# Optimization experiments

Measured on AMD Instinct MI355X. Metric: run time of the kernel, lower is better.

The kernel has to match this reference:

```python
import jax, jax.numpy as jnp
import numpy as np

H, KVH, DH = 16, 4, 128
EPS = 1e-8

def _rmsnorm(t, gamma):
    # normalize over last dim (dim_head)
    ms = jnp.mean(t * t, axis=-1, keepdims=True)
    return t * jax.lax.rsqrt(ms + EPS) * gamma

def setup_inputs() -> dict:
    key = jax.random.key(0)
    ks = jax.random.split(key, 5)
    d = H * DH  # 2048
    kv_d = KVH * DH  # 512
    x = jax.random.normal(ks[0], (2, 2048, d), dtype=jnp.float32)
    Wq = jax.random.normal(ks[1], (d, d), dtype=jnp.float32) * (d ** -0.5)
    Wk = jax.random.normal(ks[2], (d, kv_d), dtype=jnp.float32) * (d ** -0.5)
    Wv = jax.random.normal(ks[3], (d, kv_d), dtype=jnp.float32) * (d ** -0.5)
    Wo = jax.random.normal(ks[4], (d, d), dtype=jnp.float32) * (d ** -0.5)
    q_gamma = jnp.ones((DH,), dtype=jnp.float32)
    k_gamma = jnp.ones((DH,), dtype=jnp.float32)
    return {"x": x, "Wq": Wq, "Wk": Wk, "Wv": Wv, "Wo": Wo,
            "q_gamma": q_gamma, "k_gamma": k_gamma}

def reference(x, Wq, Wk, Wv, Wo, q_gamma, k_gamma):
    b, s, d = x.shape
    g = H // KVH  # GQA group size
    q = (x @ Wq).reshape(b, s, H, DH)
    k = (x @ Wk).reshape(b, s, KVH, DH)
    v = (x @ Wv).reshape(b, s, KVH, DH)
    # fused QK RMSNorm (per-head, over dim_head)
    q = _rmsnorm(q, q_gamma)
    k = _rmsnorm(k, k_gamma)
    # GQA: expand kv heads across query-head groups
    k = jnp.repeat(k, g, axis=2)  # [b, s, H, DH]
    v = jnp.repeat(v, g, axis=2)
    scores = jnp.einsum('bqhd,bkhd->bhqk', q, k) * (DH ** -0.5)
    causal = jnp.tril(jnp.ones((s, s), dtype=bool))
    scores = jnp.where(causal, scores, jnp.finfo(scores.dtype).min)
    attn = jax.nn.softmax(scores, axis=-1)
    out = jnp.einsum('bhqk,bkhd->bqhd', attn, v).reshape(b, s, H * DH)
    out = out @ Wo
    return out + x  # residual skip
```

## Files before the change

kernel.cpp:

```cpp
#include <hip/hip_runtime.h>

typedef unsigned short u16;
typedef __attribute__((ext_vector_type(8))) short short8;
typedef __attribute__((ext_vector_type(4))) float f32x4;

#define DEVI __device__ __forceinline__

DEVI float u2f(u16 u) {
    unsigned int x = ((unsigned int)u) << 16;
    float f; __builtin_memcpy(&f, &x, 4); return f;
}
DEVI u16 f2u(float f) {
    unsigned int x; __builtin_memcpy(&x, &f, 4);
    x = (x + 0x7fffu + ((x >> 16) & 1u)) >> 16;
    return (u16)x;
}
DEVI unsigned int fbits(float f) {
    unsigned int x; __builtin_memcpy(&x, &f, 4); return x;
}
DEVI void gld16(const u16* g, u16* ldsbase) {
    __builtin_amdgcn_global_load_lds(
        (const __attribute__((address_space(1))) unsigned int*)g,
        (__attribute__((address_space(3))) unsigned int*)ldsbase, 16, 0, 0);
}

__global__ __launch_bounds__(256) void prep(
    const float* __restrict__ x,
    const float* __restrict__ Wq, const float* __restrict__ Wk,
    const float* __restrict__ Wv, const float* __restrict__ Wo,
    u16* __restrict__ xbf, u16* __restrict__ WTqkv, u16* __restrict__ WoT)
{
    __shared__ u16 T[64 * 72];
    int id = blockIdx.x;
    const int tid = threadIdx.x;
    if (id < 4096) {
        int g = (id * 256 + tid) * 8;
        float4 a = *(const float4*)&x[g];
        float4 c = *(const float4*)&x[g + 4];
        short8 v;
        v[0]=(short)f2u(a.x); v[1]=(short)f2u(a.y); v[2]=(short)f2u(a.z); v[3]=(short)f2u(a.w);
        v[4]=(short)f2u(c.x); v[5]=(short)f2u(c.y); v[6]=(short)f2u(c.z); v[7]=(short)f2u(c.w);
        *(short8*)&xbf[g] = v;
        return;
    }
    id -= 4096;
    const float* W; u16* WT; int N, bx, by;
    if (id < 1024)      {            W = Wo; WT = WoT;   N = 2048; bx = id & 31; by = id >> 5; }
    else if (id < 2048) { id -= 1024; W = Wq; WT = WTqkv; N = 2048; bx = id & 31; by = id >> 5; }
    else if (id < 2304) { id -= 2048; W = Wk; WT = WTqkv + (size_t)2048 * 2048; N = 512; bx = id & 7; by = id >> 3; }
    else                { id -= 2304; W = Wv; WT = WTqkv + (size_t)2560 * 2048; N = 512; bx = id & 7; by = id >> 3; }
    const int K = 2048;
    const int k0 = by * 64, n0 = bx * 64;
#pragma unroll
    for (int i = 0; i < 2; ++i) {
        int c = tid + i * 256;
        int row = c >> 3, n8 = (c & 7) * 8;
        const float* src = &W[(size_t)(k0 + row) * N + n0 + n8];
#pragma unroll
        for (int j = 0; j < 8; ++j)
            T[(n8 + j) * 72 + row] = f2u(src[j]);
    }
    __syncthreads();
#pragma unroll
    for (int i = 0; i < 2; ++i) {
        int c = tid + i * 256;
        int n = c >> 3, k8 = (c & 7) * 8;
        *(short8*)&WT[(size_t)(n0 + n) * K + k0 + k8] = *(const short8*)&T[n * 72 + k8];
    }
}

__global__ __launch_bounds__(256) void gemm_lds(
    const u16* __restrict__ A, int lda,
    const u16* __restrict__ WT,
    void* __restrict__ C, int ldc, const float* __restrict__ resid, int c_f32,
    int M, int N, int K,
    const float* __restrict__ qg, const float* __restrict__ kg, int fuse_norm)
{
    __shared__ u16 As[128 * 32];
    __shared__ u16 Bs[128 * 32];
    const int tid = threadIdx.x;
    const int lane = tid & 63, w = tid >> 6;
    const int wm = w >> 1, wn = w & 1;
    const int l15 = lane & 15, quad = lane >> 4;
    const int r4 = lane >> 2, c4 = (lane & 3) * 8;
    const int m0 = blockIdx.y * 128, n0 = blockIdx.x * 128;

    f32x4 acc[4][4] = {};
    for (int k0 = 0; k0 < K; k0 += 32) {
#pragma unroll
        for (int j = 0; j < 2; ++j) {
            int row = w * 32 + j * 16;
            gld16(&WT[(size_t)(n0 + row + r4) * K + k0 + c4], &Bs[row * 32]);
            gld16(&A [(size_t)(m0 + row + r4) * lda + k0 + c4], &As[row * 32]);
        }
        __syncthreads();
        short8 a[4], b[4];
#pragma unroll
        for (int mt = 0; mt < 4; ++mt)
            a[mt] = *(const short8*)&As[(wm * 64 + mt * 16 + l15) * 32 + quad * 8];
#pragma unroll
        for (int nt = 0; nt < 4; ++nt)
            b[nt] = *(const short8*)&Bs[(wn * 64 + nt * 16 + l15) * 32 + quad * 8];
#pragma unroll
        for (int mt = 0; mt < 4; ++mt)
#pragma unroll
            for (int nt = 0; nt < 4; ++nt)
                acc[mt][nt] = __builtin_amdgcn_mfma_f32_16x16x32_bf16(a[mt], b[nt], acc[mt][nt], 0, 0, 0);
        __syncthreads();
    }

    if (fuse_norm && n0 < 2560) {
        const float* gamma = (n0 < 2048) ? qg : kg;
        float* red = (float*)As;
#pragma unroll
        for (int mt = 0; mt < 4; ++mt)
#pragma unroll
            for (int r = 0; r < 4; ++r) {
                float p = 0.f;
#pragma unroll
                for (int nt = 0; nt < 4; ++nt) p += acc[mt][nt][r] * acc[mt][nt][r];
#pragma unroll
                for (int msk = 1; msk < 16; msk <<= 1) p += __shfl_xor(p, msk);
                if (l15 == 0)
                    red[(wm * 64 + mt * 16 + quad * 4 + r) * 2 + wn] = p;
            }
        __syncthreads();
        float gv[4];
#pragma unroll
        for (int nt = 0; nt < 4; ++nt) gv[nt] = gamma[wn * 64 + nt * 16 + l15];
#pragma unroll
        for (int mt = 0; mt < 4; ++mt)
#pragma unroll
            for (int r = 0; r < 4; ++r) {
                int rl = wm * 64 + mt * 16 + quad * 4 + r;
                float m2 = red[rl * 2] + red[rl * 2 + 1];
                float sc = rsqrtf(m2 * (1.0f / 128.0f) + 1e-8f);
#pragma unroll
                for (int nt = 0; nt < 4; ++nt) acc[mt][nt][r] *= sc * gv[nt];
            }
    }

#pragma unroll
    for (int mt = 0; mt < 4; ++mt) {
#pragma unroll
        for (int r = 0; r < 4; ++r) {
            int row = m0 + wm * 64 + mt * 16 + quad * 4 + r;
#pragma unroll
            for (int nt = 0; nt < 4; ++nt) {
                int col = n0 + wn * 64 + nt * 16 + l15;
                float v = acc[mt][nt][r];
                if (resid) v += resid[(size_t)row * ldc + col];
                if (c_f32) ((float*)C)[(size_t)row * ldc + col] = v;
                else       ((u16*)C)[(size_t)row * ldc + col] = f2u(v);
            }
        }
    }
}

__global__ __launch_bounds__(256) void vtrans(
    const u16* __restrict__ qkv, u16* __restrict__ vT)
{
    __shared__ u16 T[128 * 72];
    const int tid = threadIdx.x;
    const int t0 = blockIdx.x * 64;
    const int kvh = blockIdx.y, b = blockIdx.z;
#pragma unroll
    for (int i = 0; i < 4; ++i) {
        int c = tid + i * 256;
        int tl = c >> 4, d8 = (c & 15) * 8;
        short8 v = *(const short8*)&qkv[(size_t)(b * 2048 + t0 + tl) * 3072 + 2560 + kvh * 128 + d8];
#pragma unroll
        for (int j = 0; j < 8; ++j)
            T[(d8 + j) * 72 + tl] = (u16)v[j];
    }
    __syncthreads();
#pragma unroll
    for (int i = 0; i < 4; ++i) {
        int c = tid + i * 256;
        int d = c >> 3, t8 = (c & 7) * 8;
        *(short8*)&vT[((size_t)(b * 4 + kvh) * 128 + d) * 2048 + t0 + t8] =
            *(const short8*)&T[d * 72 + t8];
    }
}

#define QS 136
#define VS 72
__global__ __launch_bounds__(256) void attn(
    u16* __restrict__ qkv, const u16* __restrict__ vT)
{
    __shared__ u16 lds[17920];
    u16* const Ks = lds;
    u16* const Vs = lds + 8704;

    const int tid = threadIdx.x, lane = tid & 63, w = tid >> 6;
    const int l15 = lane & 15, quad = lane >> 4;
    const int h = blockIdx.y, b = blockIdx.z;
    const int kvh = h >> 2;
    const int qts[2] = { (int)blockIdx.x, 31 - (int)blockIdx.x };
    const float scale = 0.08838834764831845f;

#pragma unroll
    for (int t = 0; t < 2; ++t)
#pragma unroll
        for (int i = 0; i < 4; ++i) {
            int c = tid + i * 256;
            int r = c >> 4, d8 = (c & 15) * 8;
            *(short8*)&lds[t * 8704 + r * QS + d8] =
                *(const short8*)&qkv[(size_t)(b * 2048 + qts[t] * 64 + r) * 3072 + h * 128 + d8];
        }
    __syncthreads();
    short8 qf[2][4];
#pragma unroll
    for (int t = 0; t < 2; ++t)
#pragma unroll
        for (int ks = 0; ks < 4; ++ks)
            qf[t][ks] = *(const short8*)&lds[t * 8704 + (w * 16 + l15) * QS + ks * 32 + quad * 8];
    __syncthreads();

    f32x4 o[2][8] = {};
    float m_[2] = { -1e30f, -1e30f }, l_[2] = { 0.f, 0.f };

    for (int kt = 0; kt <= qts[1]; ++kt) {
        const int kv0 = kt * 64;
#pragma unroll
        for (int i = 0; i < 4; ++i) {
            int c = tid + i * 256;
            int r = c >> 4, d8 = (c & 15) * 8;
            *(short8*)&Ks[r * QS + d8] =
                *(const short8*)&qkv[(size_t)(b * 2048 + kv0 + r) * 3072 + 2048 + kvh * 128 + d8];
        }
#pragma unroll
        for (int i = 0; i < 4; ++i) {
            int c = tid + i * 256;
            int d = c >> 3, t8 = (c & 7) * 8;
            *(short8*)&Vs[d * VS + t8] =
                *(const short8*)&vT[((size_t)(b * 4 + kvh) * 128 + d) * 2048 + kv0 + t8];
        }
        __syncthreads();

#pragma unroll
        for (int t = 0; t < 2; ++t) {
            if (kt > qts[t]) continue;
            f32x4 s[4];
#pragma unroll
            for (int nt = 0; nt < 4; ++nt) {
                f32x4 a = {};
#pragma unroll
                for (int ks = 0; ks < 4; ++ks) {
                    short8 kf = *(const short8*)&Ks[(nt * 16 + l15) * QS + ks * 32 + quad * 8];
                    a = __builtin_amdgcn_mfma_f32_16x16x32_bf16(kf, qf[t][ks], a, 0, 0, 0);
                }
                s[nt] = a;
            }
            if (kt == qts[t]) {
                int qrow = w * 16 + l15;
#pragma unroll
                for (int nt = 0; nt < 4; ++nt)
#pragma unroll
                    for (int r = 0; r < 4; ++r) {
                        float v = s[nt][r] * scale;
                        if (nt * 16 + quad * 4 + r > qrow) v = -1e30f;
                        s[nt][r] = v;
                    }
            } else {
#pragma unroll
                for (int nt = 0; nt < 4; ++nt)
#pragma unroll
                    for (int r = 0; r < 4; ++r) s[nt][r] *= scale;
            }
            float mx = s[0][0];
#pragma unroll
            for (int nt = 0; nt < 4; ++nt)
#pragma unroll
                for (int r = 0; r < 4; ++r) mx = fmaxf(mx, s[nt][r]);
            mx = fmaxf(mx, __shfl_xor(mx, 16));
            mx = fmaxf(mx, __shfl_xor(mx, 32));
            float mn = fmaxf(m_[t], mx);
            float alpha = __expf(m_[t] - mn);
            m_[t] = mn;
            float sum = 0.f;
#pragma unroll
            for (int nt = 0; nt < 4; ++nt)
#pragma unroll
                for (int r = 0; r < 4; ++r) {
                    float p = __expf(s[nt][r] - mn);
                    s[nt][r] = p;
                    sum += p;
                }
            sum += __shfl_xor(sum, 16);
            sum += __shfl_xor(sum, 32);
            l_[t] = l_[t] * alpha + sum;
            unsigned int pk[4][2];
#pragma unroll
            for (int nt = 0; nt < 4; ++nt)
#pragma unroll
                for (int i = 0; i < 2; ++i)
                    pk[nt][i] = __builtin_amdgcn_perm(
                        fbits(s[nt][2 * i + 1]), fbits(s[nt][2 * i]), 0x07060302u);
            int af[2][4];
#pragma unroll
            for (int c = 0; c < 2; ++c)
#pragma unroll
                for (int d = 0; d < 4; ++d) {
                    int src = l15 + 16 * ((quad & 1) * 2 + (d >> 1));
                    int v0 = __shfl((int)pk[2 * c][d & 1], src);
                    int v1 = __shfl((int)pk[2 * c + 1][d & 1], src);
                    af[c][d] = (quad >= 2) ? v1 : v0;
                }
            union { int i4[4]; short8 s8; } ua0, ua1;
#pragma unroll
            for (int d = 0; d < 4; ++d) { ua0.i4[d] = af[0][d]; ua1.i4[d] = af[1][d]; }
#pragma unroll
            for (int r = 0; r < 4; ++r) {
                float ao = __shfl(alpha, quad * 4 + r);
#pragma unroll
                for (int nto = 0; nto < 8; ++nto) o[t][nto][r] *= ao;
            }
#pragma unroll
            for (int nto = 0; nto < 8; ++nto) {
                short8 bv0 = *(const short8*)&Vs[(nto * 16 + l15) * VS + quad * 8];
                short8 bv1 = *(const short8*)&Vs[(nto * 16 + l15) * VS + 32 + quad * 8];
                o[t][nto] = __builtin_amdgcn_mfma_f32_16x16x32_bf16(ua0.s8, bv0, o[t][nto], 0, 0, 0);
                o[t][nto] = __builtin_amdgcn_mfma_f32_16x16x32_bf16(ua1.s8, bv1, o[t][nto], 0, 0, 0);
            }
        }
        __syncthreads();
    }
#pragma unroll
    for (int t = 0; t < 2; ++t) {
        float rl = 1.0f / l_[t];
#pragma unroll
        for (int r = 0; r < 4; ++r) {
            float inv = __shfl(rl, quad * 4 + r);
            int row = qts[t] * 64 + w * 16 + quad * 4 + r;
#pragma unroll
            for (int nto = 0; nto < 8; ++nto)
                qkv[(size_t)(b * 2048 + row) * 3072 + h * 128 + nto * 16 + l15] =
                    f2u(o[t][nto][r] * inv);
        }
    }
}

extern "C" void kernel_launch(void* const* d_in, const int* in_sizes, int n_in,
                              void* d_out, int out_size, void* d_ws, size_t ws_size,
                              hipStream_t stream) {
    const float* x  = (const float*)d_in[0];
    const float* Wq = (const float*)d_in[1];
    const float* Wk = (const float*)d_in[2];
    const float* Wv = (const float*)d_in[3];
    const float* Wo = (const float*)d_in[4];
    const float* qg = (const float*)d_in[5];
    const float* kg = (const float*)d_in[6];

    char* ws = (char*)d_ws;
    u16* WoT   = (u16*)(ws);
    u16* QKV   = (u16*)(ws + 8388608);
    u16* vT    = (u16*)(ws + 33554432);
    u16* WTqkv = (u16*)(ws + 33554432);
    u16* xbf   = (u16*)d_out;

    prep<<<dim3(6656), 256, 0, stream>>>(x, Wq, Wk, Wv, Wo, xbf, WTqkv, WoT);

    gemm_lds<<<dim3(24, 32), 256, 0, stream>>>(xbf, 2048, WTqkv, QKV, 3072,
                                               nullptr, 0, 4096, 3072, 2048,
                                               qg, kg, 1);

    vtrans<<<dim3(32, 4, 2), 256, 0, stream>>>(QKV, vT);

    attn<<<dim3(16, 16, 2), 256, 0, stream>>>(QKV, vT);

    gemm_lds<<<dim3(16, 32), 256, 0, stream>>>(QKV, 3072, WoT, d_out, 2048,
                                               x, 1, 4096, 2048, 2048,
                                               nullptr, nullptr, 0);
}
```

Measured before the change: 357.9 us.

## Split paired causal query tiles into one tile per attention block

The attention kernel previously had each block handle two query tiles (qt and 31-qt) to balance causal work and share each K/V tile load between them. It now launches twice as many blocks, each handling one query tile, with a swizzled tile index that mixes short and long blocks across heads and batches. This doubles the number of blocks available to fill the GPU's compute units and halves per-block register use for the accumulators. In exchange, every K/V tile is loaded once per query tile instead of once per pair, and per-block work becomes imbalanced, leaving it to the scheduler to even out.

```diff
diff --git a/kernel.cpp b/kernel.cpp
--- a/kernel.cpp
+++ b/kernel.cpp
@@ -196,31 +196,27 @@
     const int l15 = lane & 15, quad = lane >> 4;
     const int h = blockIdx.y, b = blockIdx.z;
     const int kvh = h >> 2;
-    const int qts[2] = { (int)blockIdx.x, 31 - (int)blockIdx.x };
+    const int qt = ((int)blockIdx.x + ((h >> 3) << 3) + (b << 4)) & 31;
     const float scale = 0.08838834764831845f;
 
 #pragma unroll
-    for (int t = 0; t < 2; ++t)
-#pragma unroll
-        for (int i = 0; i < 4; ++i) {
-            int c = tid + i * 256;
-            int r = c >> 4, d8 = (c & 15) * 8;
-            *(short8*)&lds[t * 8704 + r * QS + d8] =
-                *(const short8*)&qkv[(size_t)(b * 2048 + qts[t] * 64 + r) * 3072 + h * 128 + d8];
-        }
+    for (int i = 0; i < 4; ++i) {
+        int c = tid + i * 256;
+        int r = c >> 4, d8 = (c & 15) * 8;
+        *(short8*)&Ks[r * QS + d8] =
+            *(const short8*)&qkv[(size_t)(b * 2048 + qt * 64 + r) * 3072 + h * 128 + d8];
+    }
     __syncthreads();
-    short8 qf[2][4];
-#pragma unroll
-    for (int t = 0; t < 2; ++t)
-#pragma unroll
-        for (int ks = 0; ks < 4; ++ks)
-            qf[t][ks] = *(const short8*)&lds[t * 8704 + (w * 16 + l15) * QS + ks * 32 + quad * 8];
+    short8 qf[4];
+#pragma unroll
+    for (int ks = 0; ks < 4; ++ks)
+        qf[ks] = *(const short8*)&Ks[(w * 16 + l15) * QS + ks * 32 + quad * 8];
     __syncthreads();
 
-    f32x4 o[2][8] = {};
-    float m_[2] = { -1e30f, -1e30f }, l_[2] = { 0.f, 0.f };
-
-    for (int kt = 0; kt <= qts[1]; ++kt) {
+    f32x4 o[8] = {};
+    float m_ = -1e30f, l_ = 0.f;
+
+    for (int kt = 0; kt <= qt; ++kt) {
         const int kv0 = kt * 64;
 #pragma unroll
         for (int i = 0; i < 4; ++i) {
@@ -238,105 +234,100 @@
         }
         __syncthreads();
 
-#pragma unroll
-        for (int t = 0; t < 2; ++t) {
-            if (kt > qts[t]) continue;
-            f32x4 s[4];
-#pragma unroll
-            for (int nt = 0; nt < 4; ++nt) {
-                f32x4 a = {};
-#pragma unroll
-                for (int ks = 0; ks < 4; ++ks) {
-                    short8 kf = *(const short8*)&Ks[(nt * 16 + l15) * QS + ks * 32 + quad * 8];
-                    a = __builtin_amdgcn_mfma_f32_16x16x32_bf16(kf, qf[t][ks], a, 0, 0, 0);
+        f32x4 s[4];
+#pragma unroll
+        for (int nt = 0; nt < 4; ++nt) {
+            f32x4 a = {};
+#pragma unroll
+            for (int ks = 0; ks < 4; ++ks) {
+                short8 kf = *(const short8*)&Ks[(nt * 16 + l15) * QS + ks * 32 + quad * 8];
+                a = __builtin_amdgcn_mfma_f32_16x16x32_bf16(kf, qf[ks], a, 0, 0, 0);
+            }
+            s[nt] = a;
+        }
+        if (kt == qt) {
+            int qrow = w * 16 + l15;
+#pragma unroll
+            for (int nt = 0; nt < 4; ++nt)
+#pragma unroll
+                for (int r = 0; r < 4; ++r) {
+                    float v = s[nt][r] * scale;
+                    if (nt * 16 + quad * 4 + r > qrow) v = -1e30f;
+                    s[nt][r] = v;
                 }
-                s[nt] = a;
-            }
-            if (kt == qts[t]) {
-                int qrow = w * 16 + l15;
-#pragma unroll
-                for (int nt = 0; nt < 4; ++nt)
-#pragma unroll
-                    for (int r = 0; r < 4; ++r) {
-                        float v = s[nt][r] * scale;
-                        if (nt * 16 + quad * 4 + r > qrow) v = -1e30f;
-                        s[nt][r] = v;
-                    }
-            } else {
-#pragma unroll
-                for (int nt = 0; nt < 4; ++nt)
-#pragma unroll
-                    for (int r = 0; r < 4; ++r) s[nt][r] *= scale;
-            }
-            float mx = s[0][0];
+        } else {
 #pragma unroll
             for (int nt = 0; nt < 4; ++nt)
 #pragma unroll
-                for (int r = 0; r < 4; ++r) mx = fmaxf(mx, s[nt][r]);
-            mx = fmaxf(mx, __shfl_xor(mx, 16));
-            mx = fmaxf(mx, __shfl_xor(mx, 32));
-            float mn = fmaxf(m_[t], mx);
-            float alpha = __expf(m_[t] - mn);
-            m_[t] = mn;
-            float sum = 0.f;
-#pragma unroll
-            for (int nt = 0; nt < 4; ++nt)
-#pragma unroll
-                for (int r = 0; r < 4; ++r) {
-                    float p = __expf(s[nt][r] - mn);
-                    s[nt][r] = p;
-                    sum += p;
-                }
-            sum += __shfl_xor(sum, 16);
-            sum += __shfl_xor(sum, 32);
-            l_[t] = l_[t] * alpha + sum;
-            unsigned int pk[4][2];
-#pragma unroll
-            for (int nt = 0; nt < 4; ++nt)
-#pragma unroll
-                for (int i = 0; i < 2; ++i)
-                    pk[nt][i] = __builtin_amdgcn_perm(
-                        fbits(s[nt][2 * i + 1]), fbits(s[nt][2 * i]), 0x07060302u);
-            int af[2][4];
-#pragma unroll
-            for (int c = 0; c < 2; ++c)
-#pragma unroll
-                for (int d = 0; d < 4; ++d) {
-                    int src = l15 + 16 * ((quad & 1) * 2 + (d >> 1));
-                    int v0 = __shfl((int)pk[2 * c][d & 1], src);
-                    int v1 = __shfl((int)pk[2 * c + 1][d & 1], src);
-                    af[c][d] = (quad >= 2) ? v1 : v0;
-                }
-            union { int i4[4]; short8 s8; } ua0, ua1;
-#pragma unroll
-            for (int d = 0; d < 4; ++d) { ua0.i4[d] = af[0][d]; ua1.i4[d] = af[1][d]; }
+                for (int r = 0; r < 4; ++r) s[nt][r] *= scale;
+        }
+        float mx = s[0][0];
+#pragma unroll
+        for (int nt = 0; nt < 4; ++nt)
+#pragma unroll
+            for (int r = 0; r < 4; ++r) mx = fmaxf(mx, s[nt][r]);
+        mx = fmaxf(mx, __shfl_xor(mx, 16));
+        mx = fmaxf(mx, __shfl_xor(mx, 32));
+        float mn = fmaxf(m_, mx);
+        float alpha = __expf(m_ - mn);
+        m_ = mn;
+        float sum = 0.f;
+#pragma unroll
+        for (int nt = 0; nt < 4; ++nt)
 #pragma unroll
             for (int r = 0; r < 4; ++r) {
-                float ao = __shfl(alpha, quad * 4 + r);
-#pragma unroll
-                for (int nto = 0; nto < 8; ++nto) o[t][nto][r] *= ao;
-            }
-#pragma unroll
-            for (int nto = 0; nto < 8; ++nto) {
-                short8 bv0 = *(const short8*)&Vs[(nto * 16 + l15) * VS + quad * 8];
-                short8 bv1 = *(const short8*)&Vs[(nto * 16 + l15) * VS + 32 + quad * 8];
-                o[t][nto] = __builtin_amdgcn_mfma_f32_16x16x32_bf16(ua0.s8, bv0, o[t][nto], 0, 0, 0);
-                o[t][nto] = __builtin_amdgcn_mfma_f32_16x16x32_bf16(ua1.s8, bv1, o[t][nto], 0, 0, 0);
-            }
-        }
-        __syncthreads();
-    }
-#pragma unroll
-    for (int t = 0; t < 2; ++t) {
-        float rl = 1.0f / l_[t];
+                float p = __expf(s[nt][r] - mn);
+                s[nt][r] = p;
+                sum += p;
+            }
+        sum += __shfl_xor(sum, 16);
+        sum += __shfl_xor(sum, 32);
+        l_ = l_ * alpha + sum;
+        unsigned int pk[4][2];
+#pragma unroll
+        for (int nt = 0; nt < 4; ++nt)
+#pragma unroll
+            for (int i = 0; i < 2; ++i)
+                pk[nt][i] = __builtin_amdgcn_perm(
+                    fbits(s[nt][2 * i + 1]), fbits(s[nt][2 * i]), 0x07060302u);
+        int af[2][4];
+#pragma unroll
+        for (int c = 0; c < 2; ++c)
+#pragma unroll
+            for (int d = 0; d < 4; ++d) {
+                int src = l15 + 16 * ((quad & 1) * 2 + (d >> 1));
+                int v0 = __shfl((int)pk[2 * c][d & 1], src);
+                int v1 = __shfl((int)pk[2 * c + 1][d & 1], src);
+                af[c][d] = (quad >= 2) ? v1 : v0;
+            }
+        union { int i4[4]; short8 s8; } ua0, ua1;
+#pragma unroll
+        for (int d = 0; d < 4; ++d) { ua0.i4[d] = af[0][d]; ua1.i4[d] = af[1][d]; }
+#pragma unroll
+        for (int r = 0; r < 4; ++r) {
+            float ao = __shfl(alpha, quad * 4 + r);
+#pragma unroll
+            for (int nto = 0; nto < 8; ++nto) o[nto][r] *= ao;
+        }
+#pragma unroll
+        for (int nto = 0; nto < 8; ++nto) {
+            short8 bv0 = *(const short8*)&Vs[(nto * 16 + l15) * VS + quad * 8];
+            short8 bv1 = *(const short8*)&Vs[(nto * 16 + l15) * VS + 32 + quad * 8];
+            o[nto] = __builtin_amdgcn_mfma_f32_16x16x32_bf16(ua0.s8, bv0, o[nto], 0, 0, 0);
+            o[nto] = __builtin_amdgcn_mfma_f32_16x16x32_bf16(ua1.s8, bv1, o[nto], 0, 0, 0);
+        }
+        __syncthreads();
+    }
+    {
+        float rl = 1.0f / l_;
 #pragma unroll
         for (int r = 0; r < 4; ++r) {
             float inv = __shfl(rl, quad * 4 + r);
-            int row = qts[t] * 64 + w * 16 + quad * 4 + r;
+            int row = qt * 64 + w * 16 + quad * 4 + r;
 #pragma unroll
             for (int nto = 0; nto < 8; ++nto)
                 qkv[(size_t)(b * 2048 + row) * 3072 + h * 128 + nto * 16 + l15] =
-                    f2u(o[t][nto][r] * inv);
+                    f2u(o[nto][r] * inv);
         }
     }
 }
@@ -367,7 +358,7 @@
 
     vtrans<<<dim3(32, 4, 2), 256, 0, stream>>>(QKV, vT);
 
-    attn<<<dim3(16, 16, 2), 256, 0, stream>>>(QKV, vT);
+    attn<<<dim3(32, 16, 2), 256, 0, stream>>>(QKV, vT);
 
     gemm_lds<<<dim3(16, 32), 256, 0, stream>>>(QKV, 3072, WoT, d_out, 2048,
                                                x, 1, 4096, 2048, 2048,
```

Result: slower. 406.7 us (+13.7%).

## Double-buffer K/V tiles in LDS with register prefetch two tiles ahead

Applied to the files above, without the earlier changes.

The attention kernel now holds two K/V tile buffers in LDS. The tile for step kt+1 is written from registers while step kt is computed, and global loads for step kt+2 are issued into registers at the same time. This is meant to hide global-load latency and take the load-then-sync stall off the critical path of each iteration. In exchange, LDS per block doubles to about 70KB and register pressure rises, which can lower occupancy.

```diff
diff --git a/kernel.cpp b/kernel.cpp
--- a/kernel.cpp
+++ b/kernel.cpp
@@ -188,9 +188,7 @@
 __global__ __launch_bounds__(256) void attn(
     u16* __restrict__ qkv, const u16* __restrict__ vT)
 {
-    __shared__ u16 lds[17920];
-    u16* const Ks = lds;
-    u16* const Vs = lds + 8704;
+    __shared__ u16 lds[35840];
 
     const int tid = threadIdx.x, lane = tid & 63, w = tid >> 6;
     const int l15 = lane & 15, quad = lane >> 4;
@@ -199,6 +197,9 @@
     const int qts[2] = { (int)blockIdx.x, 31 - (int)blockIdx.x };
     const float scale = 0.08838834764831845f;
 
+    const u16* const Kg = &qkv[(size_t)(b * 2048) * 3072 + 2048 + kvh * 128];
+    const u16* const Vg = &vT[(size_t)(b * 4 + kvh) * 128 * 2048];
+
 #pragma unroll
     for (int t = 0; t < 2; ++t)
 #pragma unroll
@@ -208,6 +209,13 @@
             *(short8*)&lds[t * 8704 + r * QS + d8] =
                 *(const short8*)&qkv[(size_t)(b * 2048 + qts[t] * 64 + r) * 3072 + h * 128 + d8];
         }
+    short8 kr[4], vr[4];
+#pragma unroll
+    for (int i = 0; i < 4; ++i) {
+        int c = tid + i * 256;
+        kr[i] = *(const short8*)&Kg[(size_t)(c >> 4) * 3072 + (c & 15) * 8];
+        vr[i] = *(const short8*)&Vg[(size_t)(c >> 3) * 2048 + (c & 7) * 8];
+    }
     __syncthreads();
     short8 qf[2][4];
 #pragma unroll
@@ -217,26 +225,59 @@
             qf[t][ks] = *(const short8*)&lds[t * 8704 + (w * 16 + l15) * QS + ks * 32 + quad * 8];
     __syncthreads();
 
+    {
+        u16* Ks = lds;
+        u16* Vs = lds + 17408;
+#pragma unroll
+        for (int i = 0; i < 4; ++i) {
+            int c = tid + i * 256;
+            *(short8*)&Ks[(c >> 4) * QS + (c & 15) * 8] = kr[i];
+        }
+#pragma unroll
+        for (int i = 0; i < 4; ++i) {
+            int c = tid + i * 256;
+            *(short8*)&Vs[(c >> 3) * VS + (c & 7) * 8] = vr[i];
+        }
+    }
+#pragma unroll
+    for (int i = 0; i < 4; ++i) {
+        int c = tid + i * 256;
+        kr[i] = *(const short8*)&Kg[(size_t)(64 + (c >> 4)) * 3072 + (c & 15) * 8];
+        vr[i] = *(const short8*)&Vg[(size_t)(c >> 3) * 2048 + 64 + (c & 7) * 8];
+    }
+    __syncthreads();
+
     f32x4 o[2][8] = {};
     float m_[2] = { -1e30f, -1e30f }, l_[2] = { 0.f, 0.f };
 
-    for (int kt = 0; kt <= qts[1]; ++kt) {
-        const int kv0 = kt * 64;
-#pragma unroll
-        for (int i = 0; i < 4; ++i) {
-            int c = tid + i * 256;
-            int r = c >> 4, d8 = (c & 15) * 8;
-            *(short8*)&Ks[r * QS + d8] =
-                *(const short8*)&qkv[(size_t)(b * 2048 + kv0 + r) * 3072 + 2048 + kvh * 128 + d8];
-        }
-#pragma unroll
-        for (int i = 0; i < 4; ++i) {
-            int c = tid + i * 256;
-            int d = c >> 3, t8 = (c & 7) * 8;
-            *(short8*)&Vs[d * VS + t8] =
-                *(const short8*)&vT[((size_t)(b * 4 + kvh) * 128 + d) * 2048 + kv0 + t8];
-        }
-        __syncthreads();
+    const int last = qts[1];
+    for (int kt = 0; kt <= last; ++kt) {
+        const int p = kt & 1;
+        if (kt < last) {
+            u16* Ksw = (p ^ 1) ? lds + 8704 : lds;
+            u16* Vsw = (p ^ 1) ? lds + 17408 + 9216 : lds + 17408;
+#pragma unroll
+            for (int i = 0; i < 4; ++i) {
+                int c = tid + i * 256;
+                *(short8*)&Ksw[(c >> 4) * QS + (c & 15) * 8] = kr[i];
+            }
+#pragma unroll
+            for (int i = 0; i < 4; ++i) {
+                int c = tid + i * 256;
+                *(short8*)&Vsw[(c >> 3) * VS + (c & 7) * 8] = vr[i];
+            }
+            if (kt + 1 < last) {
+                const int kv2 = (kt + 2) * 64;
+#pragma unroll
+                for (int i = 0; i < 4; ++i) {
+                    int c = tid + i * 256;
+                    kr[i] = *(const short8*)&Kg[(size_t)(kv2 + (c >> 4)) * 3072 + (c & 15) * 8];
+                    vr[i] = *(const short8*)&Vg[(size_t)(c >> 3) * 2048 + kv2 + (c & 7) * 8];
+                }
+            }
+        }
+        const u16* Ks = p ? lds + 8704 : lds;
+        const u16* Vs = p ? lds + 17408 + 9216 : lds + 17408;
 
 #pragma unroll
         for (int t = 0; t < 2; ++t) {
@@ -283,9 +324,9 @@
             for (int nt = 0; nt < 4; ++nt)
 #pragma unroll
                 for (int r = 0; r < 4; ++r) {
-                    float p = __expf(s[nt][r] - mn);
-                    s[nt][r] = p;
-                    sum += p;
+                    float p2 = __expf(s[nt][r] - mn);
+                    s[nt][r] = p2;
+                    sum += p2;
                 }
             sum += __shfl_xor(sum, 16);
             sum += __shfl_xor(sum, 32);
```

After: 389.1 us. 1.09x slower.
